# Optimization experiments

Measured on AMD Instinct MI355X. Metric: run time of the kernel, lower is better.

The kernel has to match this reference:

```python
import jax, jax.numpy as jnp
import numpy as np

NUM_GRAPHS = 512

def gcn_conv(x, W, b, src, dst, num_nodes):
    # PyG GCNConv: h = x @ W; add self-loops; symmetric norm D^-1/2 A D^-1/2; + bias
    h = x @ W  # [N, F]
    ones = jnp.ones(src.shape[0], dtype=x.dtype)
    deg = jax.ops.segment_sum(ones, dst, num_segments=num_nodes) + 1.0  # +1 for self-loop
    dinv = jax.lax.rsqrt(deg)  # deg >= 1 always
    coef = dinv[src] * dinv[dst]  # [E]
    msg = h[src] * coef[:, None]  # [E, F]  (dominant memory traffic)
    agg = jax.ops.segment_sum(msg, dst, num_segments=num_nodes)
    agg = agg + h * (dinv * dinv)[:, None]  # self-loop term, norm = dinv_i^2
    return agg + b

def global_mean_pool(x, batch, num_graphs):
    s = jax.ops.segment_sum(x, batch, num_segments=num_graphs)
    cnt = jax.ops.segment_sum(jnp.ones(x.shape[0], dtype=x.dtype), batch, num_segments=num_graphs)
    return s / jnp.maximum(cnt, 1.0)[:, None]

def setup_inputs() -> dict:
    key = jax.random.key(0)
    ks = jax.random.split(key, 8)
    N, E, D, H, C = 100000, 3200000, 128, 64, 2
    x = jax.random.normal(ks[0], (N, D), dtype=jnp.float32)
    edge_index = jax.random.randint(ks[1], (2, E), 0, N, dtype=jnp.int32)
    batch = jnp.sort(jax.random.randint(ks[2], (N,), 0, NUM_GRAPHS, dtype=jnp.int32))
    W1 = jax.random.normal(ks[3], (D, H), dtype=jnp.float32) / np.sqrt(D)
    b1 = jnp.zeros((H,), dtype=jnp.float32)
    W2 = jax.random.normal(ks[4], (H, H), dtype=jnp.float32) / np.sqrt(H)
    b2 = jnp.zeros((H,), dtype=jnp.float32)
    Wlin = jax.random.normal(ks[5], (H, C), dtype=jnp.float32) / np.sqrt(H)
    blin = jnp.zeros((C,), dtype=jnp.float32)
    return {"x": x, "edge_index": edge_index, "batch": batch,
            "W1": W1, "b1": b1, "W2": W2, "b2": b2, "Wlin": Wlin, "blin": blin}

def reference(x, edge_index, batch, W1, b1, W2, b2, Wlin, blin):
    # Dropout is identity at inference; omitted for a deterministic reference.
    num_nodes = x.shape[0]
    src, dst = edge_index[0], edge_index[1]
    h = jax.nn.relu(gcn_conv(x, W1, b1, src, dst, num_nodes))
    h = jax.nn.relu(gcn_conv(h, W2, b2, src, dst, num_nodes))
    g = global_mean_pool(h, batch, NUM_GRAPHS)  # [G, H]
    return g @ Wlin + blin  # [G, 2]
```

## Files before the change

### kernel.cpp

```cpp
#include <hip/hip_runtime.h>

#define HF 64

__global__ void hist_kernel(const int* __restrict__ dst, int* __restrict__ deg, int E) {
    int e = blockIdx.x * blockDim.x + threadIdx.x;
    if (e < E) atomicAdd(&deg[dst[e]], 1);
}

__global__ __launch_bounds__(256) void scan_partial(const int* __restrict__ deg,
                                                    int* __restrict__ blocksum, int N) {
    __shared__ int red[256];
    int base = blockIdx.x * 1024 + threadIdx.x * 4;
    int s = 0;
#pragma unroll
    for (int j = 0; j < 4; ++j) {
        int i = base + j;
        if (i < N) s += deg[i];
    }
    red[threadIdx.x] = s;
    __syncthreads();
    for (int o = 128; o > 0; o >>= 1) {
        if (threadIdx.x < o) red[threadIdx.x] += red[threadIdx.x + o];
        __syncthreads();
    }
    if (threadIdx.x == 0) blocksum[blockIdx.x] = red[0];
}

__global__ __launch_bounds__(256) void scan_blocksums(int* __restrict__ blocksum, int nb) {
    __shared__ int lds[256];
    int t = threadIdx.x;
    int v = (t < nb) ? blocksum[t] : 0;
    lds[t] = v;
    __syncthreads();
    for (int o = 1; o < 256; o <<= 1) {
        int add = (t >= o) ? lds[t - o] : 0;
        __syncthreads();
        lds[t] += add;
        __syncthreads();
    }
    if (t < nb) blocksum[t] = lds[t] - v;
}

__global__ __launch_bounds__(256) void scan_apply(const int* __restrict__ deg,
                                                  const int* __restrict__ blocksum,
                                                  int* __restrict__ cursor,
                                                  float* __restrict__ dinv, int N) {
    __shared__ int lds[256];
    int base = blockIdx.x * 1024 + threadIdx.x * 4;
    int v[4];
    int s = 0;
#pragma unroll
    for (int j = 0; j < 4; ++j) {
        int i = base + j;
        v[j] = (i < N) ? deg[i] : 0;
        s += v[j];
    }
    lds[threadIdx.x] = s;
    __syncthreads();
    for (int o = 1; o < 256; o <<= 1) {
        int add = (threadIdx.x >= o) ? lds[threadIdx.x - o] : 0;
        __syncthreads();
        lds[threadIdx.x] += add;
        __syncthreads();
    }
    int run = blocksum[blockIdx.x] + lds[threadIdx.x] - s;
#pragma unroll
    for (int j = 0; j < 4; ++j) {
        int i = base + j;
        if (i < N) {
            cursor[i] = run;
            dinv[i] = rsqrtf((float)v[j] + 1.0f);
            run += v[j];
        }
    }
}

__global__ void fill_kernel(const int* __restrict__ src, const int* __restrict__ dst,
                            int* __restrict__ cursor, int* __restrict__ csr_src, int E) {
    int e = blockIdx.x * blockDim.x + threadIdx.x;
    if (e < E) {
        int d = dst[e];
        int pos = atomicAdd(&cursor[d], 1);
        csr_src[pos] = src[e];
    }
}

template <int K>
__global__ __launch_bounds__(256) void gemm_scale_kernel(const float* __restrict__ X,
                                                         const float* __restrict__ W,
                                                         const float* __restrict__ scale,
                                                         float* __restrict__ Y, int N) {
    __shared__ float Wl[K * HF];
    __shared__ float xs[32 * K];
    for (int i = threadIdx.x; i < K * HF; i += 256) Wl[i] = W[i];

    int node0 = blockIdx.x * 32;
    const float4* X4 = (const float4*)(X + (size_t)node0 * K);
    float4* xs4 = (float4*)xs;
    int totalf4 = 32 * K / 4;
    for (int i = threadIdx.x; i < totalf4; i += 256) {
        int n = i / (K / 4);
        if (node0 + n < N) xs4[i] = X4[i];
    }
    __syncthreads();

    int wave = threadIdx.x >> 6, f = threadIdx.x & 63;
    for (int n = wave; n < 32; n += 4) {
        int node = node0 + n;
        if (node >= N) break;
        const float4* xr = (const float4*)&xs[n * K];
        float acc = 0.0f;
#pragma unroll
        for (int k4 = 0; k4 < K / 4; ++k4) {
            float4 xv = xr[k4];
            acc += xv.x * Wl[(k4 * 4 + 0) * HF + f];
            acc += xv.y * Wl[(k4 * 4 + 1) * HF + f];
            acc += xv.z * Wl[(k4 * 4 + 2) * HF + f];
            acc += xv.w * Wl[(k4 * 4 + 3) * HF + f];
        }
        Y[(size_t)node * HF + f] = acc * scale[node];
    }
}

__device__ __forceinline__ float edge_gather_sum(const float* __restrict__ hs,
                                                 const int* __restrict__ csr_src,
                                                 int beg, int end, int f) {
    float acc = 0.0f;
    for (int base = beg; base < end; base += 32) {
        int li = base + (f & 31);
        int myidx = csr_src[li < end ? li : beg];
        int rem = end - base;
#pragma unroll
        for (int j = 0; j < 32; ++j) {
            int s = __builtin_amdgcn_readlane(myidx, j);
            float v = hs[(size_t)s * HF + f];
            acc += (j < rem) ? v : 0.0f;
        }
    }
    return acc;
}

__global__ __launch_bounds__(256) void agg_relu_kernel(const float* __restrict__ hs,
                                                       const int* __restrict__ cursor,
                                                       const int* __restrict__ deg,
                                                       const int* __restrict__ csr_src,
                                                       const float* __restrict__ dinv,
                                                       const float* __restrict__ b,
                                                       float* __restrict__ out, int N) {
    int d = blockIdx.x * 4 + (threadIdx.x >> 6);
    if (d >= N) return;
    int f = threadIdx.x & 63;
    int end = cursor[d];
    int beg = end - deg[d];
    float acc = edge_gather_sum(hs, csr_src, beg, end, f);
    float v = dinv[d] * (acc + hs[(size_t)d * HF + f]) + b[f];
    out[(size_t)d * HF + f] = fmaxf(v, 0.0f);
}

__global__ __launch_bounds__(256) void agg_pool_kernel(const float* __restrict__ hs,
                                                       const int* __restrict__ cursor,
                                                       const int* __restrict__ deg,
                                                       const int* __restrict__ csr_src,
                                                       const float* __restrict__ dinv,
                                                       const float* __restrict__ b,
                                                       const int* __restrict__ batch,
                                                       float* __restrict__ pool,
                                                       float* __restrict__ cnt, int N) {
    int d = blockIdx.x * 4 + (threadIdx.x >> 6);
    if (d >= N) return;
    int f = threadIdx.x & 63;
    int end = cursor[d];
    int beg = end - deg[d];
    float acc = edge_gather_sum(hs, csr_src, beg, end, f);
    float v = fmaxf(dinv[d] * (acc + hs[(size_t)d * HF + f]) + b[f], 0.0f);
    int g = batch[d];
    atomicAdd(&pool[g * HF + f], v);
    if (f == 0) atomicAdd(&cnt[g], 1.0f);
}

__global__ void final_kernel(const float* __restrict__ pool, const float* __restrict__ cnt,
                             const float* __restrict__ Wlin, const float* __restrict__ blin,
                             float* __restrict__ out) {
    int g = blockIdx.x;
    int f = threadIdx.x;
    float v = pool[g * HF + f] / fmaxf(cnt[g], 1.0f);
    float s0 = v * Wlin[f * 2 + 0];
    float s1 = v * Wlin[f * 2 + 1];
#pragma unroll
    for (int off = 32; off > 0; off >>= 1) {
        s0 += __shfl_down(s0, off);
        s1 += __shfl_down(s1, off);
    }
    if (f == 0) {
        out[g * 2 + 0] = s0 + blin[0];
        out[g * 2 + 1] = s1 + blin[1];
    }
}

extern "C" void kernel_launch(void* const* d_in, const int* in_sizes, int n_in,
                              void* d_out, int out_size, void* d_ws, size_t ws_size,
                              hipStream_t stream) {
    const float* x    = (const float*)d_in[0];
    const int*   ei   = (const int*)d_in[1];
    const int*   bat  = (const int*)d_in[2];
    const float* W1   = (const float*)d_in[3];
    const float* b1   = (const float*)d_in[4];
    const float* W2   = (const float*)d_in[5];
    const float* b2   = (const float*)d_in[6];
    const float* Wlin = (const float*)d_in[7];
    const float* blin = (const float*)d_in[8];

    const int N = in_sizes[2];
    const int E = in_sizes[1] / 2;
    const int G = out_size / 2;
    const int* src  = ei;
    const int* dstv = ei + E;

    int*   deg      = (int*)d_ws;
    int*   cursor   = deg + N;
    int*   blocksum = cursor + N;
    int*   csr_src  = blocksum + 256;
    float* dinv     = (float*)(csr_src + E);
    float* bufA     = dinv + N;
    float* bufB     = bufA + (size_t)N * HF;
    float* pool     = bufB + (size_t)N * HF;
    float* cnt      = pool + (size_t)G * HF;

    int nb = (N + 1023) / 1024;

    hipMemsetAsync(deg, 0, (size_t)N * sizeof(int), stream);
    hist_kernel<<<(E + 255) / 256, 256, 0, stream>>>(dstv, deg, E);
    scan_partial<<<nb, 256, 0, stream>>>(deg, blocksum, N);
    scan_blocksums<<<1, 256, 0, stream>>>(blocksum, nb);
    scan_apply<<<nb, 256, 0, stream>>>(deg, blocksum, cursor, dinv, N);
    fill_kernel<<<(E + 255) / 256, 256, 0, stream>>>(src, dstv, cursor, csr_src, E);

    gemm_scale_kernel<128><<<(N + 31) / 32, 256, 0, stream>>>(x, W1, dinv, bufA, N);
    agg_relu_kernel<<<(N + 3) / 4, 256, 0, stream>>>(bufA, cursor, deg, csr_src, dinv, b1,
                                                     bufB, N);

    gemm_scale_kernel<64><<<(N + 31) / 32, 256, 0, stream>>>(bufB, W2, dinv, bufA, N);
    hipMemsetAsync(pool, 0, ((size_t)G * HF + G) * sizeof(float), stream);
    agg_pool_kernel<<<(N + 3) / 4, 256, 0, stream>>>(bufA, cursor, deg, csr_src, dinv, b2,
                                                     bat, pool, cnt, N);

    final_kernel<<<G, HF, 0, stream>>>(pool, cnt, Wlin, blin, (float*)d_out);
}
```

Measured before the change: 983.1 us.

## Store intermediate node features in bf16 to halve gather traffic

Intermediate feature buffers (the transformed features and the layer-1 output) are stored as bf16 instead of fp32, with conversion on load and round-to-nearest-even on store. The edge gather in both aggregation kernels then reads half as many bytes per neighbor, which targets the dominant random-access memory traffic. A separate bf16-input GEMM is added for layer 2. Accumulation stays in fp32, but rounding the stored features costs accuracy, and each lane now issues 2-byte loads, which coalesce less well per instruction.

New measurement: 976.5 us. No clear change (-0.7%).

```diff
diff --git a/kernel.cpp b/kernel.cpp
--- a/kernel.cpp
+++ b/kernel.cpp
@@ -1,6 +1,16 @@
 #include <hip/hip_runtime.h>
 
 #define HF 64
+typedef unsigned short bfraw;
+
+__device__ __forceinline__ float bf2f(bfraw u) {
+    return __uint_as_float((unsigned)u << 16);
+}
+__device__ __forceinline__ bfraw f2bf(float f) {
+    unsigned u = __float_as_uint(f);
+    unsigned r = (u + 0x7FFFu + ((u >> 16) & 1u)) >> 16;
+    return (bfraw)r;
+}
 
 __global__ void hist_kernel(const int* __restrict__ dst, int* __restrict__ deg, int E) {
     int e = blockIdx.x * blockDim.x + threadIdx.x;
@@ -86,10 +96,10 @@
 }
 
 template <int K>
-__global__ __launch_bounds__(256) void gemm_scale_kernel(const float* __restrict__ X,
-                                                         const float* __restrict__ W,
-                                                         const float* __restrict__ scale,
-                                                         float* __restrict__ Y, int N) {
+__global__ __launch_bounds__(256) void gemm_scale_f32_kernel(const float* __restrict__ X,
+                                                             const float* __restrict__ W,
+                                                             const float* __restrict__ scale,
+                                                             bfraw* __restrict__ Y, int N) {
     __shared__ float Wl[K * HF];
     __shared__ float xs[32 * K];
     for (int i = threadIdx.x; i < K * HF; i += 256) Wl[i] = W[i];
@@ -118,11 +128,49 @@
             acc += xv.z * Wl[(k4 * 4 + 2) * HF + f];
             acc += xv.w * Wl[(k4 * 4 + 3) * HF + f];
         }
-        Y[(size_t)node * HF + f] = acc * scale[node];
-    }
-}
-
-__device__ __forceinline__ float edge_gather_sum(const float* __restrict__ hs,
+        Y[(size_t)node * HF + f] = f2bf(acc * scale[node]);
+    }
+}
+
+__global__ __launch_bounds__(256) void gemm_scale_bf16_kernel(const bfraw* __restrict__ X,
+                                                              const float* __restrict__ W,
+                                                              const float* __restrict__ scale,
+                                                              bfraw* __restrict__ Y, int N) {
+    __shared__ float Wl[HF * HF];
+    __shared__ float xs[32 * HF];
+    for (int i = threadIdx.x; i < HF * HF; i += 256) Wl[i] = W[i];
+
+    int node0 = blockIdx.x * 32;
+    const ushort4* X4 = (const ushort4*)(X + (size_t)node0 * HF);
+    for (int i = threadIdx.x; i < 32 * HF / 4; i += 256) {
+        int n = i >> 4;
+        if (node0 + n < N) {
+            ushort4 u = X4[i];
+            float4 fv = make_float4(bf2f(u.x), bf2f(u.y), bf2f(u.z), bf2f(u.w));
+            ((float4*)xs)[i] = fv;
+        }
+    }
+    __syncthreads();
+
+    int wave = threadIdx.x >> 6, f = threadIdx.x & 63;
+    for (int n = wave; n < 32; n += 4) {
+        int node = node0 + n;
+        if (node >= N) break;
+        const float4* xr = (const float4*)&xs[n * HF];
+        float acc = 0.0f;
+#pragma unroll
+        for (int k4 = 0; k4 < HF / 4; ++k4) {
+            float4 xv = xr[k4];
+            acc += xv.x * Wl[(k4 * 4 + 0) * HF + f];
+            acc += xv.y * Wl[(k4 * 4 + 1) * HF + f];
+            acc += xv.z * Wl[(k4 * 4 + 2) * HF + f];
+            acc += xv.w * Wl[(k4 * 4 + 3) * HF + f];
+        }
+        Y[(size_t)node * HF + f] = f2bf(acc * scale[node]);
+    }
+}
+
+__device__ __forceinline__ float edge_gather_sum(const bfraw* __restrict__ hs,
                                                  const int* __restrict__ csr_src,
                                                  int beg, int end, int f) {
     float acc = 0.0f;
@@ -133,31 +181,32 @@
 #pragma unroll
         for (int j = 0; j < 32; ++j) {
             int s = __builtin_amdgcn_readlane(myidx, j);
-            float v = hs[(size_t)s * HF + f];
+            float v = bf2f(hs[(size_t)s * HF + f]);
             acc += (j < rem) ? v : 0.0f;
         }
     }
     return acc;
 }
 
-__global__ __launch_bounds__(256) void agg_relu_kernel(const float* __restrict__ hs,
+__global__ __launch_bounds__(256) void agg_relu_kernel(const bfraw* __restrict__ hs,
                                                        const int* __restrict__ cursor,
                                                        const int* __restrict__ deg,
                                                        const int* __restrict__ csr_src,
                                                        const float* __restrict__ dinv,
                                                        const float* __restrict__ b,
-                                                       float* __restrict__ out, int N) {
+                                                       bfraw* __restrict__ out, int N) {
     int d = blockIdx.x * 4 + (threadIdx.x >> 6);
     if (d >= N) return;
     int f = threadIdx.x & 63;
     int end = cursor[d];
     int beg = end - deg[d];
     float acc = edge_gather_sum(hs, csr_src, beg, end, f);
-    float v = dinv[d] * (acc + hs[(size_t)d * HF + f]) + b[f];
-    out[(size_t)d * HF + f] = fmaxf(v, 0.0f);
-}
-
-__global__ __launch_bounds__(256) void agg_pool_kernel(const float* __restrict__ hs,
+    float self = bf2f(hs[(size_t)d * HF + f]);
+    float v = dinv[d] * (acc + self) + b[f];
+    out[(size_t)d * HF + f] = f2bf(fmaxf(v, 0.0f));
+}
+
+__global__ __launch_bounds__(256) void agg_pool_kernel(const bfraw* __restrict__ hs,
                                                        const int* __restrict__ cursor,
                                                        const int* __restrict__ deg,
                                                        const int* __restrict__ csr_src,
@@ -172,7 +221,8 @@
     int end = cursor[d];
     int beg = end - deg[d];
     float acc = edge_gather_sum(hs, csr_src, beg, end, f);
-    float v = fmaxf(dinv[d] * (acc + hs[(size_t)d * HF + f]) + b[f], 0.0f);
+    float self = bf2f(hs[(size_t)d * HF + f]);
+    float v = fmaxf(dinv[d] * (acc + self) + b[f], 0.0f);
     int g = batch[d];
     atomicAdd(&pool[g * HF + f], v);
     if (f == 0) atomicAdd(&cnt[g], 1.0f);
@@ -221,10 +271,12 @@
     int*   blocksum = cursor + N;
     int*   csr_src  = blocksum + 256;
     float* dinv     = (float*)(csr_src + E);
-    float* bufA     = dinv + N;
-    float* bufB     = bufA + (size_t)N * HF;
-    float* pool     = bufB + (size_t)N * HF;
+    float* pool     = dinv + N;
     float* cnt      = pool + (size_t)G * HF;
+    uintptr_t p = (uintptr_t)(cnt + G);
+    p = (p + 15) & ~(uintptr_t)15;
+    bfraw* bufT = (bfraw*)p;
+    bfraw* bufH = bufT + (size_t)N * HF;
 
     int nb = (N + 1023) / 1024;
 
@@ -235,13 +287,13 @@
     scan_apply<<<nb, 256, 0, stream>>>(deg, blocksum, cursor, dinv, N);
     fill_kernel<<<(E + 255) / 256, 256, 0, stream>>>(src, dstv, cursor, csr_src, E);
 
-    gemm_scale_kernel<128><<<(N + 31) / 32, 256, 0, stream>>>(x, W1, dinv, bufA, N);
-    agg_relu_kernel<<<(N + 3) / 4, 256, 0, stream>>>(bufA, cursor, deg, csr_src, dinv, b1,
-                                                     bufB, N);
-
-    gemm_scale_kernel<64><<<(N + 31) / 32, 256, 0, stream>>>(bufB, W2, dinv, bufA, N);
+    gemm_scale_f32_kernel<128><<<(N + 31) / 32, 256, 0, stream>>>(x, W1, dinv, bufT, N);
+    agg_relu_kernel<<<(N + 3) / 4, 256, 0, stream>>>(bufT, cursor, deg, csr_src, dinv, b1,
+                                                     bufH, N);
+
+    gemm_scale_bf16_kernel<<<(N + 31) / 32, 256, 0, stream>>>(bufH, W2, dinv, bufT, N);
     hipMemsetAsync(pool, 0, ((size_t)G * HF + G) * sizeof(float), stream);
-    agg_pool_kernel<<<(N + 3) / 4, 256, 0, stream>>>(bufA, cursor, deg, csr_src, dinv, b2,
+    agg_pool_kernel<<<(N + 3) / 4, 256, 0, stream>>>(bufT, cursor, deg, csr_src, dinv, b2,
                                                      bat, pool, cnt, N);
 
     final_kernel<<<G, HF, 0, stream>>>(pool, cnt, Wlin, blin, (float*)d_out);
```

## Stage gathered neighbor rows via global_load_lds and partition CSR fill by destination range

Applied to the files above, without the earlier changes.

The edge gather now issues global-to-LDS direct loads for each neighbor row into a per-wave shared staging buffer, waits once per chunk, and then sums from LDS. This replaces the fully unrolled predicated register loads and skips loads past the end of the chunk. The CSR fill kernel is split into 8 destination partitions, each scanning all edges but only handling destinations in its range, so atomics and writes land in a more localized region at the cost of reading dst 8 times. The workspace layout also moves pool/cnt ahead of the large buffers.

Result: faster. 940.0 us (-4.4%).

```diff
diff --git a/kernel.cpp b/kernel.cpp
--- a/kernel.cpp
+++ b/kernel.cpp
@@ -1,6 +1,10 @@
 #include <hip/hip_runtime.h>
 
 #define HF 64
+#define CHUNK 32
+
+typedef __attribute__((address_space(1))) const void gvoid;
+typedef __attribute__((address_space(3))) void lvoid;
 
 __global__ void hist_kernel(const int* __restrict__ dst, int* __restrict__ deg, int E) {
     int e = blockIdx.x * blockDim.x + threadIdx.x;
@@ -75,13 +79,21 @@
     }
 }
 
-__global__ void fill_kernel(const int* __restrict__ src, const int* __restrict__ dst,
-                            int* __restrict__ cursor, int* __restrict__ csr_src, int E) {
-    int e = blockIdx.x * blockDim.x + threadIdx.x;
-    if (e < E) {
+__global__ __launch_bounds__(256) void fill_kernel(const int* __restrict__ src,
+                                                   const int* __restrict__ dst,
+                                                   int* __restrict__ cursor,
+                                                   int* __restrict__ csr_src,
+                                                   int E, int part, int nblk) {
+    int p = blockIdx.x & 7;
+    int blk = blockIdx.x >> 3;
+    int plo = p * part;
+    int phi = plo + part;
+    for (int e = blk * 256 + threadIdx.x; e < E; e += nblk * 256) {
         int d = dst[e];
-        int pos = atomicAdd(&cursor[d], 1);
-        csr_src[pos] = src[e];
+        if (d >= plo && d < phi) {
+            int pos = atomicAdd(&cursor[d], 1);
+            csr_src[pos] = src[e];
+        }
     }
 }
 
@@ -124,18 +136,22 @@
 
 __device__ __forceinline__ float edge_gather_sum(const float* __restrict__ hs,
                                                  const int* __restrict__ csr_src,
-                                                 int beg, int end, int f) {
+                                                 int beg, int end, int lane,
+                                                 float* __restrict__ wstage) {
     float acc = 0.0f;
-    for (int base = beg; base < end; base += 32) {
-        int li = base + (f & 31);
+    for (int base = beg; base < end; base += CHUNK) {
+        int li = base + (lane & 31);
         int myidx = csr_src[li < end ? li : beg];
         int rem = end - base;
-#pragma unroll
-        for (int j = 0; j < 32; ++j) {
+        if (rem > CHUNK) rem = CHUNK;
+        for (int j = 0; j < rem; ++j) {
             int s = __builtin_amdgcn_readlane(myidx, j);
-            float v = hs[(size_t)s * HF + f];
-            acc += (j < rem) ? v : 0.0f;
-        }
+            const float* gp = hs + (size_t)s * HF + lane;
+            __builtin_amdgcn_global_load_lds((gvoid*)gp, (lvoid*)(wstage + j * HF), 4, 0, 0);
+        }
+        asm volatile("s_waitcnt vmcnt(0)" ::: "memory");
+        for (int j = 0; j < rem; ++j) acc += wstage[j * HF + lane];
+        asm volatile("s_waitcnt lgkmcnt(0)" ::: "memory");
     }
     return acc;
 }
@@ -147,12 +163,14 @@
                                                        const float* __restrict__ dinv,
                                                        const float* __restrict__ b,
                                                        float* __restrict__ out, int N) {
-    int d = blockIdx.x * 4 + (threadIdx.x >> 6);
+    __shared__ float stage[4][CHUNK * HF];
+    int wave = threadIdx.x >> 6;
+    int d = blockIdx.x * 4 + wave;
     if (d >= N) return;
     int f = threadIdx.x & 63;
     int end = cursor[d];
     int beg = end - deg[d];
-    float acc = edge_gather_sum(hs, csr_src, beg, end, f);
+    float acc = edge_gather_sum(hs, csr_src, beg, end, f, stage[wave]);
     float v = dinv[d] * (acc + hs[(size_t)d * HF + f]) + b[f];
     out[(size_t)d * HF + f] = fmaxf(v, 0.0f);
 }
@@ -166,12 +184,14 @@
                                                        const int* __restrict__ batch,
                                                        float* __restrict__ pool,
                                                        float* __restrict__ cnt, int N) {
-    int d = blockIdx.x * 4 + (threadIdx.x >> 6);
+    __shared__ float stage[4][CHUNK * HF];
+    int wave = threadIdx.x >> 6;
+    int d = blockIdx.x * 4 + wave;
     if (d >= N) return;
     int f = threadIdx.x & 63;
     int end = cursor[d];
     int beg = end - deg[d];
-    float acc = edge_gather_sum(hs, csr_src, beg, end, f);
+    float acc = edge_gather_sum(hs, csr_src, beg, end, f, stage[wave]);
     float v = fmaxf(dinv[d] * (acc + hs[(size_t)d * HF + f]) + b[f], 0.0f);
     int g = batch[d];
     atomicAdd(&pool[g * HF + f], v);
@@ -221,10 +241,10 @@
     int*   blocksum = cursor + N;
     int*   csr_src  = blocksum + 256;
     float* dinv     = (float*)(csr_src + E);
-    float* bufA     = dinv + N;
+    float* pool     = dinv + N;
+    float* cnt      = pool + (size_t)G * HF;
+    float* bufA     = cnt + G;
     float* bufB     = bufA + (size_t)N * HF;
-    float* pool     = bufB + (size_t)N * HF;
-    float* cnt      = pool + (size_t)G * HF;
 
     int nb = (N + 1023) / 1024;
 
@@ -233,7 +253,9 @@
     scan_partial<<<nb, 256, 0, stream>>>(deg, blocksum, N);
     scan_blocksums<<<1, 256, 0, stream>>>(blocksum, nb);
     scan_apply<<<nb, 256, 0, stream>>>(deg, blocksum, cursor, dinv, N);
-    fill_kernel<<<(E + 255) / 256, 256, 0, stream>>>(src, dstv, cursor, csr_src, E);
+    const int part = (N + 7) / 8;
+    const int nblk = 512;
+    fill_kernel<<<8 * nblk, 256, 0, stream>>>(src, dstv, cursor, csr_src, E, part, nblk);
 
     gemm_scale_kernel<128><<<(N + 31) / 32, 256, 0, stream>>>(x, W1, dinv, bufA, N);
     agg_relu_kernel<<<(N + 3) / 4, 256, 0, stream>>>(bufA, cursor, deg, csr_src, dinv, b1,
```
